# Optimization experiments

Hardware: AMD Instinct MI355X
Metric: run time of the kernel (lower is better)

The kernel has to match this reference:

```python
import jax, jax.numpy as jnp
import numpy as np

N = 50000      # num_nodes
E = 800000     # num_edges (avg degree 16)
F_IN = 128     # num_features
H = 64         # hidden dim (fixed in module code)
C = 16         # num_classes
R = 8          # num_relations
BN_EPS = 1e-5


def setup_inputs() -> dict:
    key = jax.random.key(0)
    ks = jax.random.split(key, 16)
    s = 0.05
    f32 = jnp.float32
    inp = {
        "x": jax.random.normal(ks[0], (N, F_IN), f32),
        "edge_index": jax.random.randint(ks[1], (2, E), 0, N, dtype=jnp.int32),
        "edge_type": jax.random.randint(ks[2], (E,), 0, R, dtype=jnp.int32),
        # RGCNConv layer 1: per-relation weights, root weight, bias
        "W1": jax.random.normal(ks[3], (R, F_IN, H), f32) * s,
        "root1": jax.random.normal(ks[4], (F_IN, H), f32) * s,
        "b1": jnp.zeros((H,), f32),
        # RGCNConv layer 2
        "W2": jax.random.normal(ks[5], (R, H, H), f32) * s,
        "root2": jax.random.normal(ks[6], (H, H), f32) * s,
        "b2": jnp.zeros((H,), f32),
        # RGCNConv layer 3
        "W3": jax.random.normal(ks[7], (R, H, H), f32) * s,
        "root3": jax.random.normal(ks[8], (H, H), f32) * s,
        "b3": jnp.zeros((H,), f32),
        # BatchNorm1d params + running stats (eval mode)
        "gamma1": jnp.ones((H,), f32), "beta1": jnp.zeros((H,), f32),
        "rm1": jnp.zeros((H,), f32),   "rv1": jnp.ones((H,), f32),
        "gamma2": jnp.ones((H,), f32), "beta2": jnp.zeros((H,), f32),
        "rm2": jnp.zeros((H,), f32),   "rv2": jnp.ones((H,), f32),
        "gamma3": jnp.ones((H,), f32), "beta3": jnp.zeros((H,), f32),
        "rm3": jnp.zeros((H,), f32),   "rv3": jnp.ones((H,), f32),
        # final linear
        "Wl": jax.random.normal(ks[9], (H, C), f32) * s,
        "bl": jnp.zeros((C,), f32),
    }
    return inp


def _rgcn(x, src, dst, edge_type, W, root, bias):
    # RGCNConv with mean aggregation per relation (PyG default):
    # out_i = x_i @ root + bias + sum_r mean_{j in N_r(i)} (x_j @ W_r)
    out = x @ root + bias
    for r in range(R):  # small fixed loop over relations
        h = x @ W[r]                      # [N, H] node-level transform
        mask = (edge_type == r)
        msg = jnp.where(mask[:, None], h[src], 0.0)   # [E, H]
        agg = jax.ops.segment_sum(msg, dst, num_segments=N)   # [N, H]
        cnt = jax.ops.segment_sum(mask.astype(x.dtype), dst, num_segments=N)
        out = out + agg / jnp.maximum(cnt, 1.0)[:, None]
    return out


def _bn(x, gamma, beta, rm, rv):
    # BatchNorm1d in eval mode with running stats
    return (x - rm) * jax.lax.rsqrt(rv + BN_EPS) * gamma + beta


def reference(x, edge_index, edge_type,
              W1, root1, b1, W2, root2, b2, W3, root3, b3,
              gamma1, beta1, rm1, rv1,
              gamma2, beta2, rm2, rv2,
              gamma3, beta3, rm3, rv3,
              Wl, bl):
    src, dst = edge_index[0], edge_index[1]
    h = jax.nn.relu(_rgcn(x, src, dst, edge_type, W1, root1, b1))
    h = _bn(h, gamma1, beta1, rm1, rv1)  # dropout = identity in eval
    h = jax.nn.relu(_rgcn(h, src, dst, edge_type, W2, root2, b2))
    h = _bn(h, gamma2, beta2, rm2, rv2)
    h = jax.nn.relu(_rgcn(h, src, dst, edge_type, W3, root3, b3))
    h = _bn(h, gamma3, beta3, rm3, rv3)
    return h @ Wl + bl  # [N, C]
```

## Files before the change

### kernel.cpp

```cpp
#include <hip/hip_runtime.h>


#define R_REL 8

typedef unsigned short ushort_t;
typedef short short8 __attribute__((ext_vector_type(8)));
typedef float f32x4 __attribute__((ext_vector_type(4)));

#define MFMA(a, b, c) __builtin_amdgcn_mfma_f32_16x16x32_bf16(a, b, c, 0, 0, 0)

static __device__ __forceinline__ unsigned short f2bf(float f) {
    unsigned int u = __float_as_uint(f);
    u = (u + 0x7FFF + ((u >> 16) & 1)) >> 16;
    return (unsigned short)u;
}
static __device__ __forceinline__ float bf2f(unsigned short h) {
    return __uint_as_float(((unsigned int)h) << 16);
}

__global__ void wcvt_kernel(const float* __restrict__ src, ushort_t* __restrict__ dst,
                            int G, int K)
{
    int i = blockIdx.x * 256 + threadIdx.x;
    if (i >= G * K * 64) return;
    int g = i / (K * 64), rem = i % (K * 64), k = rem >> 6, c = rem & 63;
    dst[(size_t)g * 64 * K + (size_t)c * K + k] = f2bf(src[i]);
}

__global__ void xcvt_kernel(const float* __restrict__ src, ushort_t* __restrict__ dst, int n4)
{
    int i = blockIdx.x * 256 + threadIdx.x;
    if (i >= n4) return;
    float4 v = ((const float4*)src)[i];
    ushort_t t[4] = {f2bf(v.x), f2bf(v.y), f2bf(v.z), f2bf(v.w)};
    *(uint2*)&dst[(size_t)i * 4] = *(const uint2*)t;
}

__global__ __launch_bounds__(256)
void mgemm_kernel(const ushort_t* __restrict__ A, int n, int K,
                  const ushort_t* __restrict__ WT, const ushort_t* __restrict__ RT,
                  const float* __restrict__ bias,
                  ushort_t* __restrict__ H, float* __restrict__ accb)
{
    __shared__ ushort_t As[64][136];
    __shared__ ushort_t Bs[64][136];

    const int row0 = blockIdx.x * 64;
    const int yr = blockIdx.y;
    const ushort_t* Bsrc = (yr < R_REL) ? (WT + (size_t)yr * 64 * K) : RT;

    const int tid = threadIdx.x;
    const int KB = K >> 3;

    for (int i = tid; i < 64 * KB; i += 256) {
        int r = i / KB, k8 = (i % KB) << 3;
        *(uint4*)&Bs[r][k8] = *(const uint4*)&Bsrc[(size_t)r * K + k8];
        uint4 av = make_uint4(0u, 0u, 0u, 0u);
        if (row0 + r < n) av = *(const uint4*)&A[(size_t)(row0 + r) * K + k8];
        *(uint4*)&As[r][k8] = av;
    }
    __syncthreads();

    const int wid  = tid >> 6;
    const int lane = tid & 63;
    const int wr = (wid >> 1) * 32;
    const int wc = (wid & 1) * 32;
    const int fr = lane & 15;
    const int kg = (lane >> 4) << 3;

    f32x4 acc[2][2] = {};
    for (int k0 = 0; k0 < K; k0 += 32) {
        short8 a0 = *(const short8*)&As[wr + fr     ][k0 + kg];
        short8 a1 = *(const short8*)&As[wr + 16 + fr][k0 + kg];
        short8 b0 = *(const short8*)&Bs[wc + fr     ][k0 + kg];
        short8 b1 = *(const short8*)&Bs[wc + 16 + fr][k0 + kg];
        acc[0][0] = MFMA(a0, b0, acc[0][0]);
        acc[0][1] = MFMA(a0, b1, acc[0][1]);
        acc[1][0] = MFMA(a1, b0, acc[1][0]);
        acc[1][1] = MFMA(a1, b1, acc[1][1]);
    }
    __syncthreads();

    float* Ct = (float*)As;
    const int rbase = (lane >> 4) << 2;
    #pragma unroll
    for (int m = 0; m < 2; ++m)
        #pragma unroll
        for (int nn = 0; nn < 2; ++nn)
            #pragma unroll
            for (int j = 0; j < 4; ++j)
                Ct[(wr + m * 16 + rbase + j) * 68 + wc + nn * 16 + fr] = acc[m][nn][j];
    __syncthreads();

    if (yr < R_REL) {
        const int cb = yr << 6;
        for (int i = tid; i < 64 * 8; i += 256) {
            int r = i >> 3, c8 = (i & 7) << 3;
            if (row0 + r < n) {
                ushort_t t[8];
                #pragma unroll
                for (int j = 0; j < 8; ++j) t[j] = f2bf(Ct[r * 68 + c8 + j]);
                *(uint4*)&H[(size_t)(row0 + r) * 512 + cb + c8] = *(const uint4*)t;
            }
        }
    } else {
        for (int i = tid; i < 64 * 16; i += 256) {
            int r = i >> 4, c4 = (i & 15) << 2;
            if (row0 + r < n) {
                float4 o;
                o.x = Ct[r * 68 + c4 + 0] + bias[c4 + 0];
                o.y = Ct[r * 68 + c4 + 1] + bias[c4 + 1];
                o.z = Ct[r * 68 + c4 + 2] + bias[c4 + 2];
                o.w = Ct[r * 68 + c4 + 3] + bias[c4 + 3];
                *(float4*)&accb[(size_t)(row0 + r) * 64 + c4] = o;
            }
        }
    }
}

__global__ void count_kernel(const int* __restrict__ ei, const int* __restrict__ et,
                             int* __restrict__ cnt, int E)
{
    int e = blockIdx.x * 256 + threadIdx.x;
    if (e < E) atomicAdd(&cnt[(size_t)ei[E + e] * R_REL + et[e]], 1);
}

__global__ void invdeg_kernel(float* __restrict__ inv, int* __restrict__ deg, int N)
{
    int i = blockIdx.x * 256 + threadIdx.x;
    if (i >= N) return;
    const int* c = (const int*)inv;
    int tot = 0;
    float out[R_REL];
    #pragma unroll
    for (int r = 0; r < R_REL; ++r) {
        int cc = c[i * R_REL + r];
        tot += cc;
        out[r] = 1.0f / (float)(cc > 1 ? cc : 1);
    }
    #pragma unroll
    for (int r = 0; r < R_REL; ++r) inv[i * R_REL + r] = out[r];
    deg[i] = tot;
}

__global__ void scan1_kernel(const int* __restrict__ deg, int* __restrict__ offs,
                             int* __restrict__ partials, int N)
{
    __shared__ int sm[256];
    int i = blockIdx.x * 256 + threadIdx.x;
    int c = (i < N) ? deg[i] : 0;
    sm[threadIdx.x] = c;
    __syncthreads();
    for (int off = 1; off < 256; off <<= 1) {
        int t = (threadIdx.x >= off) ? sm[threadIdx.x - off] : 0;
        __syncthreads();
        sm[threadIdx.x] += t;
        __syncthreads();
    }
    if (i < N) offs[i] = sm[threadIdx.x] - c;
    if (threadIdx.x == 255) partials[blockIdx.x] = sm[255];
}

__global__ void scan2_kernel(int* __restrict__ partials, int P)
{
    __shared__ int sm[256];
    __shared__ int carry;
    if (threadIdx.x == 0) carry = 0;
    __syncthreads();
    for (int base = 0; base < P; base += 256) {
        int i = base + threadIdx.x;
        int c = (i < P) ? partials[i] : 0;
        sm[threadIdx.x] = c;
        __syncthreads();
        for (int off = 1; off < 256; off <<= 1) {
            int t = (threadIdx.x >= off) ? sm[threadIdx.x - off] : 0;
            __syncthreads();
            sm[threadIdx.x] += t;
            __syncthreads();
        }
        int incl = sm[threadIdx.x];
        int cold = carry;
        if (i < P) partials[i] = incl - c + cold;
        __syncthreads();
        if (threadIdx.x == 0) carry = cold + sm[255];
        __syncthreads();
    }
}

__global__ void scan3_kernel(int* __restrict__ offs, const int* __restrict__ partials, int N)
{
    int i = blockIdx.x * 256 + threadIdx.x;
    if (i < N) offs[i] += partials[blockIdx.x];
}

__global__ void fill3_kernel(const int* __restrict__ ei, const int* __restrict__ et,
                             const int* __restrict__ offs, int* __restrict__ cursor,
                             const float* __restrict__ inv,
                             int2* __restrict__ ep, int E)
{
    int e = blockIdx.x * 256 + threadIdx.x;
    if (e >= E) return;
    int d = ei[E + e];
    int r = et[e];
    int pos = offs[d] + atomicAdd(&cursor[d], 1);
    ep[pos] = make_int2(ei[e] * 512 + r * 64,
                        __float_as_int(inv[(size_t)d * R_REL + r]));
}

__global__ __launch_bounds__(256)
void agg3_kernel(const int2* __restrict__ ep,
                 const int* __restrict__ offs, const int* __restrict__ deg,
                 const ushort_t* __restrict__ H, const float* __restrict__ accb,
                 const float* __restrict__ g, const float* __restrict__ b,
                 const float* __restrict__ rm, const float* __restrict__ rv,
                 ushort_t* __restrict__ xout, int N)
{
    const int lane = threadIdx.x & 63;
    const int d = (blockIdx.x * 256 + threadIdx.x) >> 6;
    if (d >= N) return;

    const int sub = lane >> 4;
    const int fl  = lane & 15;
    const int n0 = offs[d];
    const int dg = deg[d];

    float s0 = 0.f, s1 = 0.f, s2 = 0.f, s3 = 0.f;
    int k = 0;

    for (; k + 8 <= dg; k += 8) {
        int2 eA = ep[n0 + k + sub];
        int2 eB = ep[n0 + k + 4 + sub];
        uint2 hA = *(const uint2*)&H[(size_t)eA.x + (fl << 2)];
        uint2 hB = *(const uint2*)&H[(size_t)eB.x + (fl << 2)];
        float wA = __int_as_float(eA.y);
        float wB = __int_as_float(eB.y);
        s0 += bf2f((ushort_t)(hA.x & 0xFFFF)) * wA + bf2f((ushort_t)(hB.x & 0xFFFF)) * wB;
        s1 += bf2f((ushort_t)(hA.x >> 16))    * wA + bf2f((ushort_t)(hB.x >> 16))    * wB;
        s2 += bf2f((ushort_t)(hA.y & 0xFFFF)) * wA + bf2f((ushort_t)(hB.y & 0xFFFF)) * wB;
        s3 += bf2f((ushort_t)(hA.y >> 16))    * wA + bf2f((ushort_t)(hB.y >> 16))    * wB;
    }
    for (; k + 4 <= dg; k += 4) {
        int2 eA = ep[n0 + k + sub];
        uint2 hA = *(const uint2*)&H[(size_t)eA.x + (fl << 2)];
        float wA = __int_as_float(eA.y);
        s0 += bf2f((ushort_t)(hA.x & 0xFFFF)) * wA;
        s1 += bf2f((ushort_t)(hA.x >> 16))    * wA;
        s2 += bf2f((ushort_t)(hA.y & 0xFFFF)) * wA;
        s3 += bf2f((ushort_t)(hA.y >> 16))    * wA;
    }
    if (k < dg && sub < dg - k) {
        int2 eA = ep[n0 + k + sub];
        uint2 hA = *(const uint2*)&H[(size_t)eA.x + (fl << 2)];
        float wA = __int_as_float(eA.y);
        s0 += bf2f((ushort_t)(hA.x & 0xFFFF)) * wA;
        s1 += bf2f((ushort_t)(hA.x >> 16))    * wA;
        s2 += bf2f((ushort_t)(hA.y & 0xFFFF)) * wA;
        s3 += bf2f((ushort_t)(hA.y >> 16))    * wA;
    }

    s0 += __shfl_xor(s0, 16); s1 += __shfl_xor(s1, 16);
    s2 += __shfl_xor(s2, 16); s3 += __shfl_xor(s3, 16);
    s0 += __shfl_xor(s0, 32); s1 += __shfl_xor(s1, 32);
    s2 += __shfl_xor(s2, 32); s3 += __shfl_xor(s3, 32);

    if (sub == 0) {
        const int c4 = fl << 2;
        float4 a  = *(const float4*)&accb[(size_t)d * 64 + c4];
        float4 gm = *(const float4*)&g[c4];
        float4 bt = *(const float4*)&b[c4];
        float4 mu = *(const float4*)&rm[c4];
        float4 vr = *(const float4*)&rv[c4];
        float t0 = a.x + s0, t1 = a.y + s1, t2 = a.z + s2, t3 = a.w + s3;
        t0 = t0 > 0.f ? t0 : 0.f;  t1 = t1 > 0.f ? t1 : 0.f;
        t2 = t2 > 0.f ? t2 : 0.f;  t3 = t3 > 0.f ? t3 : 0.f;
        t0 = (t0 - mu.x) * rsqrtf(vr.x + 1e-5f) * gm.x + bt.x;
        t1 = (t1 - mu.y) * rsqrtf(vr.y + 1e-5f) * gm.y + bt.y;
        t2 = (t2 - mu.z) * rsqrtf(vr.z + 1e-5f) * gm.z + bt.z;
        t3 = (t3 - mu.w) * rsqrtf(vr.w + 1e-5f) * gm.w + bt.w;
        ushort_t o[4] = {f2bf(t0), f2bf(t1), f2bf(t2), f2bf(t3)};
        *(uint2*)&xout[(size_t)d * 64 + c4] = *(const uint2*)o;
    }
}

__global__ __launch_bounds__(256)
void lin_kernel(const ushort_t* __restrict__ h, const float* __restrict__ Wl,
                const float* __restrict__ bl, float* __restrict__ out, int N)
{
    __shared__ float w[64 * 16];
    __shared__ float bb[16];
    for (int i = threadIdx.x; i < 64 * 16; i += 256) w[i] = Wl[i];
    if (threadIdx.x < 16) bb[threadIdx.x] = bl[threadIdx.x];
    __syncthreads();

    int idx = blockIdx.x * 256 + threadIdx.x;
    if (idx >= N * 16) return;
    int node = idx >> 4, c = idx & 15;
    float s = bb[c];
    const ushort_t* hr = h + (size_t)node * 64;
    #pragma unroll 16
    for (int k = 0; k < 64; ++k) s += bf2f(hr[k]) * w[k * 16 + c];
    out[idx] = s;
}

extern "C" void kernel_launch(void* const* d_in, const int* in_sizes, int n_in,
                              void* d_out, int out_size, void* d_ws, size_t ws_size,
                              hipStream_t stream)
{
    const float* x  = (const float*)d_in[0];
    const int*   ei = (const int*)d_in[1];
    const int*   et = (const int*)d_in[2];
    const float* W[3]    = {(const float*)d_in[3], (const float*)d_in[6], (const float*)d_in[9]};
    const float* root[3] = {(const float*)d_in[4], (const float*)d_in[7], (const float*)d_in[10]};
    const float* bias[3] = {(const float*)d_in[5], (const float*)d_in[8], (const float*)d_in[11]};
    const float* gamma[3] = {(const float*)d_in[12], (const float*)d_in[16], (const float*)d_in[20]};
    const float* beta[3]  = {(const float*)d_in[13], (const float*)d_in[17], (const float*)d_in[21]};
    const float* rm[3]    = {(const float*)d_in[14], (const float*)d_in[18], (const float*)d_in[22]};
    const float* rv[3]    = {(const float*)d_in[15], (const float*)d_in[19], (const float*)d_in[23]};
    const float* Wl = (const float*)d_in[24];
    const float* bl = (const float*)d_in[25];

    const int N = in_sizes[0] / 128;
    const int E = in_sizes[2];
    const int K1 = 128;

    char* p = (char*)d_ws;
    float*   inv  = (float*)p;    p += (size_t)N * R_REL * 4;
    ushort_t* Hbuf = (ushort_t*)p; p += (size_t)N * 512 * 2;
    float*   accb = (float*)p;    p += (size_t)N * 64 * 4;
    ushort_t* xb  = (ushort_t*)p; p += (size_t)N * 64 * 2;
    ushort_t* x16 = (ushort_t*)p; p += (size_t)N * K1 * 2;
    ushort_t* wt0 = (ushort_t*)p; p += (size_t)R_REL * 64 * K1 * 2;
    ushort_t* wt1 = (ushort_t*)p; p += (size_t)R_REL * 64 * 64 * 2;
    ushort_t* wt2 = (ushort_t*)p; p += (size_t)R_REL * 64 * 64 * 2;
    ushort_t* rt0 = (ushort_t*)p; p += (size_t)64 * K1 * 2;
    ushort_t* rt1 = (ushort_t*)p; p += (size_t)64 * 64 * 2;
    ushort_t* rt2 = (ushort_t*)p; p += (size_t)64 * 64 * 2;
    int*   offs    = (int*)p;     p += (size_t)N * 4;
    int*   deg     = (int*)p;     p += (size_t)N * 4;
    int*   cursor  = (int*)p;     p += (size_t)N * 4;
    int2*  ep      = (int2*)p;    p += (size_t)E * 8;
    int*   partials = (int*)p;

    const ushort_t* wt[3] = {wt0, wt1, wt2};
    const ushort_t* rt[3] = {rt0, rt1, rt2};

    const int gxN = (N + 255) / 256;

    wcvt_kernel<<<(R_REL * K1 * 64 + 255) / 256, 256, 0, stream>>>(W[0], wt0, R_REL, K1);
    wcvt_kernel<<<(R_REL * 64 * 64 + 255) / 256, 256, 0, stream>>>(W[1], wt1, R_REL, 64);
    wcvt_kernel<<<(R_REL * 64 * 64 + 255) / 256, 256, 0, stream>>>(W[2], wt2, R_REL, 64);
    wcvt_kernel<<<(K1 * 64 + 255) / 256, 256, 0, stream>>>(root[0], rt0, 1, K1);
    wcvt_kernel<<<(64 * 64 + 255) / 256, 256, 0, stream>>>(root[1], rt1, 1, 64);
    wcvt_kernel<<<(64 * 64 + 255) / 256, 256, 0, stream>>>(root[2], rt2, 1, 64);
    xcvt_kernel<<<((N * K1 / 4) + 255) / 256, 256, 0, stream>>>(x, x16, N * K1 / 4);

    hipMemsetAsync(inv, 0, (size_t)N * R_REL * 4, stream);
    hipMemsetAsync(cursor, 0, (size_t)N * 4, stream);
    count_kernel<<<(E + 255) / 256, 256, 0, stream>>>(ei, et, (int*)inv, E);
    invdeg_kernel<<<gxN, 256, 0, stream>>>(inv, deg, N);
    scan1_kernel<<<gxN, 256, 0, stream>>>(deg, offs, partials, N);
    scan2_kernel<<<1, 256, 0, stream>>>(partials, gxN);
    scan3_kernel<<<gxN, 256, 0, stream>>>(offs, partials, N);
    fill3_kernel<<<(E + 255) / 256, 256, 0, stream>>>(ei, et, offs, cursor, inv, ep, E);

    const int gx = (N + 63) / 64;
    const int gagg = (N * 64 + 255) / 256;
    const ushort_t* cur = x16;
    for (int layer = 0; layer < 3; ++layer) {
        const int K = (layer == 0) ? K1 : 64;
        mgemm_kernel<<<dim3(gx, R_REL + 1), 256, 0, stream>>>(
            cur, N, K, wt[layer], rt[layer], bias[layer], Hbuf, accb);
        agg3_kernel<<<gagg, 256, 0, stream>>>(
            ep, offs, deg, Hbuf, accb,
            gamma[layer], beta[layer], rm[layer], rv[layer], xb, N);
        cur = xb;
    }

    lin_kernel<<<(N * 16 + 255) / 256, 256, 0, stream>>>(cur, Wl, bl, (float*)d_out, N);
}
```

Baseline: 396.5 us.

## Restructure GEMM to reuse A across relations, pack edges, fuse final linear

The relation GEMM now loads each block's A rows into registers once and loops over all 9 weight matrices, reading B directly from global memory instead of staging through LDS. Results are written straight from the MFMA accumulators, with the bias folded into the initial accumulator. Edge records shrink from 8 to 4 bytes by packing src and relation into one int and looking up the inverse degree per destination at aggregation time. The six weight-conversion launches become one, and the final linear layer is fused into the last aggregation kernel via shuffles. The packing assumes node ids fit in 16 bits, which holds for N=50000.

```diff
diff --git a/kernel.cpp b/kernel.cpp
--- a/kernel.cpp
+++ b/kernel.cpp
@@ -18,13 +18,22 @@
     return __uint_as_float(((unsigned int)h) << 16);
 }
 
-__global__ void wcvt_kernel(const float* __restrict__ src, ushort_t* __restrict__ dst,
-                            int G, int K)
+struct WcvtA {
+    const float* src[6];
+    ushort_t*    dst[6];
+    int          end[6];
+    int          K[6];
+};
+__global__ void wcvt6_kernel(WcvtA a, int total)
 {
     int i = blockIdx.x * 256 + threadIdx.x;
-    if (i >= G * K * 64) return;
-    int g = i / (K * 64), rem = i % (K * 64), k = rem >> 6, c = rem & 63;
-    dst[(size_t)g * 64 * K + (size_t)c * K + k] = f2bf(src[i]);
+    if (i >= total) return;
+    int s = 0;
+    while (i >= a.end[s]) ++s;
+    int j = i - (s ? a.end[s - 1] : 0);
+    int K = a.K[s];
+    int g = j / (K * 64), rem = j % (K * 64), k = rem >> 6, c = rem & 63;
+    a.dst[s][(size_t)g * 64 * K + (size_t)c * K + k] = f2bf(a.src[s][j]);
 }
 
 __global__ void xcvt_kernel(const float* __restrict__ src, ushort_t* __restrict__ dst, int n4)
@@ -36,83 +45,85 @@
     *(uint2*)&dst[(size_t)i * 4] = *(const uint2*)t;
 }
 
+template<int K>
 __global__ __launch_bounds__(256)
-void mgemm_kernel(const ushort_t* __restrict__ A, int n, int K,
-                  const ushort_t* __restrict__ WT, const ushort_t* __restrict__ RT,
-                  const float* __restrict__ bias,
-                  ushort_t* __restrict__ H, float* __restrict__ accb)
-{
-    __shared__ ushort_t As[64][136];
-    __shared__ ushort_t Bs[64][136];
-
-    const int row0 = blockIdx.x * 64;
-    const int yr = blockIdx.y;
-    const ushort_t* Bsrc = (yr < R_REL) ? (WT + (size_t)yr * 64 * K) : RT;
-
+void mgemm2_kernel(const ushort_t* __restrict__ A, int n,
+                   const ushort_t* __restrict__ WT, const ushort_t* __restrict__ RT,
+                   const float* __restrict__ bias,
+                   ushort_t* __restrict__ H, float* __restrict__ accb)
+{
+    constexpr int KS = K / 32;
     const int tid = threadIdx.x;
-    const int KB = K >> 3;
-
-    for (int i = tid; i < 64 * KB; i += 256) {
-        int r = i / KB, k8 = (i % KB) << 3;
-        *(uint4*)&Bs[r][k8] = *(const uint4*)&Bsrc[(size_t)r * K + k8];
-        uint4 av = make_uint4(0u, 0u, 0u, 0u);
-        if (row0 + r < n) av = *(const uint4*)&A[(size_t)(row0 + r) * K + k8];
-        *(uint4*)&As[r][k8] = av;
-    }
-    __syncthreads();
-
-    const int wid  = tid >> 6;
-    const int lane = tid & 63;
-    const int wr = (wid >> 1) * 32;
-    const int wc = (wid & 1) * 32;
+    const int wid = tid >> 6, lane = tid & 63;
+    const int wr = (wid >> 1) << 5;
+    const int wc = (wid & 1) << 5;
     const int fr = lane & 15;
     const int kg = (lane >> 4) << 3;
-
-    f32x4 acc[2][2] = {};
-    for (int k0 = 0; k0 < K; k0 += 32) {
-        short8 a0 = *(const short8*)&As[wr + fr     ][k0 + kg];
-        short8 a1 = *(const short8*)&As[wr + 16 + fr][k0 + kg];
-        short8 b0 = *(const short8*)&Bs[wc + fr     ][k0 + kg];
-        short8 b1 = *(const short8*)&Bs[wc + 16 + fr][k0 + kg];
-        acc[0][0] = MFMA(a0, b0, acc[0][0]);
-        acc[0][1] = MFMA(a0, b1, acc[0][1]);
-        acc[1][0] = MFMA(a1, b0, acc[1][0]);
-        acc[1][1] = MFMA(a1, b1, acc[1][1]);
-    }
-    __syncthreads();
-
-    float* Ct = (float*)As;
-    const int rbase = (lane >> 4) << 2;
+    const int cq = (lane >> 4) << 2;
+    const int row0 = blockIdx.x * 64;
+
+    short8 a[2][KS];
     #pragma unroll
-    for (int m = 0; m < 2; ++m)
+    for (int m = 0; m < 2; ++m) {
+        int rr = row0 + wr + m * 16 + fr;
+        if (rr < n) {
+            #pragma unroll
+            for (int ks = 0; ks < KS; ++ks)
+                a[m][ks] = *(const short8*)&A[(size_t)rr * K + ks * 32 + kg];
+        } else {
+            #pragma unroll
+            for (int ks = 0; ks < KS; ++ks)
+                a[m][ks] = short8{0, 0, 0, 0, 0, 0, 0, 0};
+        }
+    }
+
+    for (int r = 0; r < 9; ++r) {
+        const ushort_t* B = (r < R_REL) ? (WT + (size_t)r * 64 * K) : RT;
+
+        short8 b[2][KS];
         #pragma unroll
         for (int nn = 0; nn < 2; ++nn)
             #pragma unroll
-            for (int j = 0; j < 4; ++j)
-                Ct[(wr + m * 16 + rbase + j) * 68 + wc + nn * 16 + fr] = acc[m][nn][j];
-    __syncthreads();
-
-    if (yr < R_REL) {
-        const int cb = yr << 6;
-        for (int i = tid; i < 64 * 8; i += 256) {
-            int r = i >> 3, c8 = (i & 7) << 3;
-            if (row0 + r < n) {
-                ushort_t t[8];
+            for (int ks = 0; ks < KS; ++ks)
+                b[nn][ks] = *(const short8*)&B[(size_t)(wc + nn * 16 + fr) * K + ks * 32 + kg];
+
+        f32x4 acc[2][2];
+        if (r == R_REL) {
+            #pragma unroll
+            for (int nn = 0; nn < 2; ++nn) {
+                float4 bv = *(const float4*)&bias[wc + nn * 16 + cq];
+                acc[nn][0] = f32x4{bv.x, bv.y, bv.z, bv.w};
+                acc[nn][1] = acc[nn][0];
+            }
+        } else {
+            acc[0][0] = f32x4{0.f, 0.f, 0.f, 0.f};
+            acc[0][1] = acc[0][0]; acc[1][0] = acc[0][0]; acc[1][1] = acc[0][0];
+        }
+
+        #pragma unroll
+        for (int ks = 0; ks < KS; ++ks)
+            #pragma unroll
+            for (int nn = 0; nn < 2; ++nn)
                 #pragma unroll
-                for (int j = 0; j < 8; ++j) t[j] = f2bf(Ct[r * 68 + c8 + j]);
-                *(uint4*)&H[(size_t)(row0 + r) * 512 + cb + c8] = *(const uint4*)t;
-            }
-        }
-    } else {
-        for (int i = tid; i < 64 * 16; i += 256) {
-            int r = i >> 4, c4 = (i & 15) << 2;
-            if (row0 + r < n) {
-                float4 o;
-                o.x = Ct[r * 68 + c4 + 0] + bias[c4 + 0];
-                o.y = Ct[r * 68 + c4 + 1] + bias[c4 + 1];
-                o.z = Ct[r * 68 + c4 + 2] + bias[c4 + 2];
-                o.w = Ct[r * 68 + c4 + 3] + bias[c4 + 3];
-                *(float4*)&accb[(size_t)(row0 + r) * 64 + c4] = o;
+                for (int m = 0; m < 2; ++m)
+                    acc[nn][m] = MFMA(b[nn][ks], a[m][ks], acc[nn][m]);
+
+        #pragma unroll
+        for (int m = 0; m < 2; ++m) {
+            int rr = row0 + wr + m * 16 + fr;
+            if (rr >= n) continue;
+            #pragma unroll
+            for (int nn = 0; nn < 2; ++nn) {
+                if (r < R_REL) {
+                    ushort_t t[4] = {f2bf(acc[nn][m][0]), f2bf(acc[nn][m][1]),
+                                     f2bf(acc[nn][m][2]), f2bf(acc[nn][m][3])};
+                    *(uint2*)&H[(size_t)rr * 512 + (r << 6) + wc + nn * 16 + cq] =
+                        *(const uint2*)t;
+                } else {
+                    *(float4*)&accb[(size_t)rr * 64 + wc + nn * 16 + cq] =
+                        make_float4(acc[nn][m][0], acc[nn][m][1],
+                                    acc[nn][m][2], acc[nn][m][3]);
+                }
             }
         }
     }
@@ -193,27 +204,27 @@
     if (i < N) offs[i] += partials[blockIdx.x];
 }
 
-__global__ void fill3_kernel(const int* __restrict__ ei, const int* __restrict__ et,
+__global__ void fill4_kernel(const int* __restrict__ ei, const int* __restrict__ et,
                              const int* __restrict__ offs, int* __restrict__ cursor,
-                             const float* __restrict__ inv,
-                             int2* __restrict__ ep, int E)
+                             int* __restrict__ ep, int E)
 {
     int e = blockIdx.x * 256 + threadIdx.x;
     if (e >= E) return;
     int d = ei[E + e];
-    int r = et[e];
     int pos = offs[d] + atomicAdd(&cursor[d], 1);
-    ep[pos] = make_int2(ei[e] * 512 + r * 64,
-                        __float_as_int(inv[(size_t)d * R_REL + r]));
+    ep[pos] = ei[e] | (et[e] << 16);
 }
 
 __global__ __launch_bounds__(256)
-void agg3_kernel(const int2* __restrict__ ep,
+void agg4_kernel(const int* __restrict__ ep,
                  const int* __restrict__ offs, const int* __restrict__ deg,
                  const ushort_t* __restrict__ H, const float* __restrict__ accb,
+                 const float* __restrict__ inv,
                  const float* __restrict__ g, const float* __restrict__ b,
                  const float* __restrict__ rm, const float* __restrict__ rv,
-                 ushort_t* __restrict__ xout, int N)
+                 ushort_t* __restrict__ xout,
+                 const float* __restrict__ Wl, const float* __restrict__ bl,
+                 float* __restrict__ out, int N, int last)
 {
     const int lane = threadIdx.x & 63;
     const int d = (blockIdx.x * 256 + threadIdx.x) >> 6;
@@ -223,35 +234,36 @@
     const int fl  = lane & 15;
     const int n0 = offs[d];
     const int dg = deg[d];
+    const float* invd = &inv[(size_t)d * R_REL];
 
     float s0 = 0.f, s1 = 0.f, s2 = 0.f, s3 = 0.f;
     int k = 0;
 
     for (; k + 8 <= dg; k += 8) {
-        int2 eA = ep[n0 + k + sub];
-        int2 eB = ep[n0 + k + 4 + sub];
-        uint2 hA = *(const uint2*)&H[(size_t)eA.x + (fl << 2)];
-        uint2 hB = *(const uint2*)&H[(size_t)eB.x + (fl << 2)];
-        float wA = __int_as_float(eA.y);
-        float wB = __int_as_float(eB.y);
+        int pA = ep[n0 + k + sub];
+        int pB = ep[n0 + k + 4 + sub];
+        uint2 hA = *(const uint2*)&H[(size_t)(pA & 0xFFFF) * 512 + ((pA >> 16) << 6) + (fl << 2)];
+        uint2 hB = *(const uint2*)&H[(size_t)(pB & 0xFFFF) * 512 + ((pB >> 16) << 6) + (fl << 2)];
+        float wA = invd[pA >> 16];
+        float wB = invd[pB >> 16];
         s0 += bf2f((ushort_t)(hA.x & 0xFFFF)) * wA + bf2f((ushort_t)(hB.x & 0xFFFF)) * wB;
         s1 += bf2f((ushort_t)(hA.x >> 16))    * wA + bf2f((ushort_t)(hB.x >> 16))    * wB;
         s2 += bf2f((ushort_t)(hA.y & 0xFFFF)) * wA + bf2f((ushort_t)(hB.y & 0xFFFF)) * wB;
         s3 += bf2f((ushort_t)(hA.y >> 16))    * wA + bf2f((ushort_t)(hB.y >> 16))    * wB;
     }
     for (; k + 4 <= dg; k += 4) {
-        int2 eA = ep[n0 + k + sub];
-        uint2 hA = *(const uint2*)&H[(size_t)eA.x + (fl << 2)];
-        float wA = __int_as_float(eA.y);
+        int pA = ep[n0 + k + sub];
+        uint2 hA = *(const uint2*)&H[(size_t)(pA & 0xFFFF) * 512 + ((pA >> 16) << 6) + (fl << 2)];
+        float wA = invd[pA >> 16];
         s0 += bf2f((ushort_t)(hA.x & 0xFFFF)) * wA;
         s1 += bf2f((ushort_t)(hA.x >> 16))    * wA;
         s2 += bf2f((ushort_t)(hA.y & 0xFFFF)) * wA;
         s3 += bf2f((ushort_t)(hA.y >> 16))    * wA;
     }
     if (k < dg && sub < dg - k) {
-        int2 eA = ep[n0 + k + sub];
-        uint2 hA = *(const uint2*)&H[(size_t)eA.x + (fl << 2)];
-        float wA = __int_as_float(eA.y);
+        int pA = ep[n0 + k + sub];
+        uint2 hA = *(const uint2*)&H[(size_t)(pA & 0xFFFF) * 512 + ((pA >> 16) << 6) + (fl << 2)];
+        float wA = invd[pA >> 16];
         s0 += bf2f((ushort_t)(hA.x & 0xFFFF)) * wA;
         s1 += bf2f((ushort_t)(hA.x >> 16))    * wA;
         s2 += bf2f((ushort_t)(hA.y & 0xFFFF)) * wA;
@@ -263,43 +275,45 @@
     s0 += __shfl_xor(s0, 32); s1 += __shfl_xor(s1, 32);
     s2 += __shfl_xor(s2, 32); s3 += __shfl_xor(s3, 32);
 
-    if (sub == 0) {
-        const int c4 = fl << 2;
-        float4 a  = *(const float4*)&accb[(size_t)d * 64 + c4];
-        float4 gm = *(const float4*)&g[c4];
-        float4 bt = *(const float4*)&b[c4];
-        float4 mu = *(const float4*)&rm[c4];
-        float4 vr = *(const float4*)&rv[c4];
-        float t0 = a.x + s0, t1 = a.y + s1, t2 = a.z + s2, t3 = a.w + s3;
-        t0 = t0 > 0.f ? t0 : 0.f;  t1 = t1 > 0.f ? t1 : 0.f;
-        t2 = t2 > 0.f ? t2 : 0.f;  t3 = t3 > 0.f ? t3 : 0.f;
-        t0 = (t0 - mu.x) * rsqrtf(vr.x + 1e-5f) * gm.x + bt.x;
-        t1 = (t1 - mu.y) * rsqrtf(vr.y + 1e-5f) * gm.y + bt.y;
-        t2 = (t2 - mu.z) * rsqrtf(vr.z + 1e-5f) * gm.z + bt.z;
-        t3 = (t3 - mu.w) * rsqrtf(vr.w + 1e-5f) * gm.w + bt.w;
-        ushort_t o[4] = {f2bf(t0), f2bf(t1), f2bf(t2), f2bf(t3)};
-        *(uint2*)&xout[(size_t)d * 64 + c4] = *(const uint2*)o;
-    }
-}
-
-__global__ __launch_bounds__(256)
-void lin_kernel(const ushort_t* __restrict__ h, const float* __restrict__ Wl,
-                const float* __restrict__ bl, float* __restrict__ out, int N)
-{
-    __shared__ float w[64 * 16];
-    __shared__ float bb[16];
-    for (int i = threadIdx.x; i < 64 * 16; i += 256) w[i] = Wl[i];
-    if (threadIdx.x < 16) bb[threadIdx.x] = bl[threadIdx.x];
-    __syncthreads();
-
-    int idx = blockIdx.x * 256 + threadIdx.x;
-    if (idx >= N * 16) return;
-    int node = idx >> 4, c = idx & 15;
-    float s = bb[c];
-    const ushort_t* hr = h + (size_t)node * 64;
-    #pragma unroll 16
-    for (int k = 0; k < 64; ++k) s += bf2f(hr[k]) * w[k * 16 + c];
-    out[idx] = s;
+    const int c4 = fl << 2;
+    float4 aq = *(const float4*)&accb[(size_t)d * 64 + c4];
+    float4 gm = *(const float4*)&g[c4];
+    float4 bt = *(const float4*)&b[c4];
+    float4 mu = *(const float4*)&rm[c4];
+    float4 vr = *(const float4*)&rv[c4];
+    float t0 = aq.x + s0, t1 = aq.y + s1, t2 = aq.z + s2, t3 = aq.w + s3;
+    t0 = t0 > 0.f ? t0 : 0.f;  t1 = t1 > 0.f ? t1 : 0.f;
+    t2 = t2 > 0.f ? t2 : 0.f;  t3 = t3 > 0.f ? t3 : 0.f;
+    t0 = (t0 - mu.x) * rsqrtf(vr.x + 1e-5f) * gm.x + bt.x;
+    t1 = (t1 - mu.y) * rsqrtf(vr.y + 1e-5f) * gm.y + bt.y;
+    t2 = (t2 - mu.z) * rsqrtf(vr.z + 1e-5f) * gm.z + bt.z;
+    t3 = (t3 - mu.w) * rsqrtf(vr.w + 1e-5f) * gm.w + bt.w;
+
+    if (!last) {
+        if (sub == 0) {
+            ushort_t o[4] = {f2bf(t0), f2bf(t1), f2bf(t2), f2bf(t3)};
+            *(uint2*)&xout[(size_t)d * 64 + c4] = *(const uint2*)o;
+        }
+    } else {
+        float p0 = 0.f, p1 = 0.f, p2 = 0.f, p3 = 0.f;
+        float tt[4] = {t0, t1, t2, t3};
+        #pragma unroll
+        for (int i = 0; i < 4; ++i) {
+            float4 wv = *(const float4*)&Wl[(size_t)(c4 + i) * 16 + (sub << 2)];
+            p0 += tt[i] * wv.x; p1 += tt[i] * wv.y;
+            p2 += tt[i] * wv.z; p3 += tt[i] * wv.w;
+        }
+        #pragma unroll
+        for (int m = 1; m < 16; m <<= 1) {
+            p0 += __shfl_xor(p0, m); p1 += __shfl_xor(p1, m);
+            p2 += __shfl_xor(p2, m); p3 += __shfl_xor(p3, m);
+        }
+        if (fl == 0) {
+            float4 bv = *(const float4*)&bl[sub << 2];
+            *(float4*)&out[(size_t)d * 16 + (sub << 2)] =
+                make_float4(p0 + bv.x, p1 + bv.y, p2 + bv.z, p3 + bv.w);
+        }
+    }
 }
 
 extern "C" void kernel_launch(void* const* d_in, const int* in_sizes, int n_in,
@@ -338,7 +352,7 @@
     int*   offs    = (int*)p;     p += (size_t)N * 4;
     int*   deg     = (int*)p;     p += (size_t)N * 4;
     int*   cursor  = (int*)p;     p += (size_t)N * 4;
-    int2*  ep      = (int2*)p;    p += (size_t)E * 8;
+    int*   ep      = (int*)p;     p += (size_t)E * 4;
     int*   partials = (int*)p;
 
     const ushort_t* wt[3] = {wt0, wt1, wt2};
@@ -346,12 +360,20 @@
 
     const int gxN = (N + 255) / 256;
 
-    wcvt_kernel<<<(R_REL * K1 * 64 + 255) / 256, 256, 0, stream>>>(W[0], wt0, R_REL, K1);
-    wcvt_kernel<<<(R_REL * 64 * 64 + 255) / 256, 256, 0, stream>>>(W[1], wt1, R_REL, 64);
-    wcvt_kernel<<<(R_REL * 64 * 64 + 255) / 256, 256, 0, stream>>>(W[2], wt2, R_REL, 64);
-    wcvt_kernel<<<(K1 * 64 + 255) / 256, 256, 0, stream>>>(root[0], rt0, 1, K1);
-    wcvt_kernel<<<(64 * 64 + 255) / 256, 256, 0, stream>>>(root[1], rt1, 1, 64);
-    wcvt_kernel<<<(64 * 64 + 255) / 256, 256, 0, stream>>>(root[2], rt2, 1, 64);
+    {
+        WcvtA a;
+        a.src[0] = W[0];   a.dst[0] = wt0; a.K[0] = K1;
+        a.src[1] = W[1];   a.dst[1] = wt1; a.K[1] = 64;
+        a.src[2] = W[2];   a.dst[2] = wt2; a.K[2] = 64;
+        a.src[3] = root[0]; a.dst[3] = rt0; a.K[3] = K1;
+        a.src[4] = root[1]; a.dst[4] = rt1; a.K[4] = 64;
+        a.src[5] = root[2]; a.dst[5] = rt2; a.K[5] = 64;
+        int sizes[6] = {R_REL * K1 * 64, R_REL * 64 * 64, R_REL * 64 * 64,
+                        K1 * 64, 64 * 64, 64 * 64};
+        int acc = 0;
+        for (int i = 0; i < 6; ++i) { acc += sizes[i]; a.end[i] = acc; }
+        wcvt6_kernel<<<(acc + 255) / 256, 256, 0, stream>>>(a, acc);
+    }
     xcvt_kernel<<<((N * K1 / 4) + 255) / 256, 256, 0, stream>>>(x, x16, N * K1 / 4);
 
     hipMemsetAsync(inv, 0, (size_t)N * R_REL * 4, stream);
@@ -361,20 +383,23 @@
     scan1_kernel<<<gxN, 256, 0, stream>>>(deg, offs, partials, N);
     scan2_kernel<<<1, 256, 0, stream>>>(partials, gxN);
     scan3_kernel<<<gxN, 256, 0, stream>>>(offs, partials, N);
-    fill3_kernel<<<(E + 255) / 256, 256, 0, stream>>>(ei, et, offs, cursor, inv, ep, E);
+    fill4_kernel<<<(E + 255) / 256, 256, 0, stream>>>(ei, et, offs, cursor, ep, E);
 
     const int gx = (N + 63) / 64;
     const int gagg = (N * 64 + 255) / 256;
     const ushort_t* cur = x16;
     for (int layer = 0; layer < 3; ++layer) {
-        const int K = (layer == 0) ? K1 : 64;
-        mgemm_kernel<<<dim3(gx, R_REL + 1), 256, 0, stream>>>(
-            cur, N, K, wt[layer], rt[layer], bias[layer], Hbuf, accb);
-        agg3_kernel<<<gagg, 256, 0, stream>>>(
-            ep, offs, deg, Hbuf, accb,
-            gamma[layer], beta[layer], rm[layer], rv[layer], xb, N);
+        if (layer == 0)
+            mgemm2_kernel<128><<<gx, 256, 0, stream>>>(
+                cur, N, wt[0], rt[0], bias[0], Hbuf, accb);
+        else
+            mgemm2_kernel<64><<<gx, 256, 0, stream>>>(
+                cur, N, wt[layer], rt[layer], bias[layer], Hbuf, accb);
+        int last = (layer == 2);
+        agg4_kernel<<<gagg, 256, 0, stream>>>(
+            ep, offs, deg, Hbuf, accb, inv,
+            gamma[layer], beta[layer], rm[layer], rv[layer],
+            xb, Wl, bl, (float*)d_out, N, last);
         cur = xb;
     }
-
-    lin_kernel<<<(N * 16 + 255) / 256, 256, 0, stream>>>(cur, Wl, bl, (float*)d_out, N);
-}
+}
```

New measurement: 427.0 us. 1.08x slower.

## Fuse conversions, scan, and final linear into neighboring kernels; template GEMM on K

Applied to the files above, without the earlier changes.

Merges the six weight-conversion launches into one, folds the x fp32-to-bf16 conversion into the layer-1 GEMM load, combines invdeg with the first scan stage, and fuses the final linear layer into the last aggregation kernel using lane shuffles. The GEMM is templated on K so its inner loop fully unrolls. The aim is to cut launch count and the extra HBM round trips for x16 and the last-layer activations. The fused linear layer adds shuffle reductions to the aggregation epilogue, and the GEMM now reads x as fp32, so twice the bytes per row for layer 1.

```diff
diff --git a/kernel.cpp b/kernel.cpp
--- a/kernel.cpp
+++ b/kernel.cpp
@@ -18,26 +18,27 @@
     return __uint_as_float(((unsigned int)h) << 16);
 }
 
-__global__ void wcvt_kernel(const float* __restrict__ src, ushort_t* __restrict__ dst,
-                            int G, int K)
+struct WcvtA {
+    const float* src[6];
+    ushort_t*    dst[6];
+    int          end[6];
+    int          K[6];
+};
+__global__ void wcvt6_kernel(WcvtA a, int total)
 {
     int i = blockIdx.x * 256 + threadIdx.x;
-    if (i >= G * K * 64) return;
-    int g = i / (K * 64), rem = i % (K * 64), k = rem >> 6, c = rem & 63;
-    dst[(size_t)g * 64 * K + (size_t)c * K + k] = f2bf(src[i]);
-}
-
-__global__ void xcvt_kernel(const float* __restrict__ src, ushort_t* __restrict__ dst, int n4)
-{
-    int i = blockIdx.x * 256 + threadIdx.x;
-    if (i >= n4) return;
-    float4 v = ((const float4*)src)[i];
-    ushort_t t[4] = {f2bf(v.x), f2bf(v.y), f2bf(v.z), f2bf(v.w)};
-    *(uint2*)&dst[(size_t)i * 4] = *(const uint2*)t;
-}
-
+    if (i >= total) return;
+    int s = 0;
+    while (i >= a.end[s]) ++s;
+    int j = i - (s ? a.end[s - 1] : 0);
+    int K = a.K[s];
+    int g = j / (K * 64), rem = j % (K * 64), k = rem >> 6, c = rem & 63;
+    a.dst[s][(size_t)g * 64 * K + (size_t)c * K + k] = f2bf(a.src[s][j]);
+}
+
+template<int K, bool AF32>
 __global__ __launch_bounds__(256)
-void mgemm_kernel(const ushort_t* __restrict__ A, int n, int K,
+void mgemm_kernel(const void* __restrict__ Av, int n,
                   const ushort_t* __restrict__ WT, const ushort_t* __restrict__ RT,
                   const float* __restrict__ bias,
                   ushort_t* __restrict__ H, float* __restrict__ accb)
@@ -55,20 +56,34 @@
     for (int i = tid; i < 64 * KB; i += 256) {
         int r = i / KB, k8 = (i % KB) << 3;
         *(uint4*)&Bs[r][k8] = *(const uint4*)&Bsrc[(size_t)r * K + k8];
-        uint4 av = make_uint4(0u, 0u, 0u, 0u);
-        if (row0 + r < n) av = *(const uint4*)&A[(size_t)(row0 + r) * K + k8];
-        *(uint4*)&As[r][k8] = av;
+        if (AF32) {
+            const float* Af = (const float*)Av;
+            float4 f0 = make_float4(0.f, 0.f, 0.f, 0.f), f1 = f0;
+            if (row0 + r < n) {
+                f0 = *(const float4*)&Af[(size_t)(row0 + r) * K + k8];
+                f1 = *(const float4*)&Af[(size_t)(row0 + r) * K + k8 + 4];
+            }
+            ushort_t t[8] = {f2bf(f0.x), f2bf(f0.y), f2bf(f0.z), f2bf(f0.w),
+                             f2bf(f1.x), f2bf(f1.y), f2bf(f1.z), f2bf(f1.w)};
+            *(uint4*)&As[r][k8] = *(const uint4*)t;
+        } else {
+            const ushort_t* Ab = (const ushort_t*)Av;
+            uint4 av = make_uint4(0u, 0u, 0u, 0u);
+            if (row0 + r < n) av = *(const uint4*)&Ab[(size_t)(row0 + r) * K + k8];
+            *(uint4*)&As[r][k8] = av;
+        }
     }
     __syncthreads();
 
     const int wid  = tid >> 6;
     const int lane = tid & 63;
-    const int wr = (wid >> 1) * 32;
-    const int wc = (wid & 1) * 32;
+    const int wr = (wid >> 1) << 5;
+    const int wc = (wid & 1) << 5;
     const int fr = lane & 15;
     const int kg = (lane >> 4) << 3;
 
     f32x4 acc[2][2] = {};
+    #pragma unroll
     for (int k0 = 0; k0 < K; k0 += 32) {
         short8 a0 = *(const short8*)&As[wr + fr     ][k0 + kg];
         short8 a1 = *(const short8*)&As[wr + 16 + fr][k0 + kg];
@@ -125,31 +140,27 @@
     if (e < E) atomicAdd(&cnt[(size_t)ei[E + e] * R_REL + et[e]], 1);
 }
 
-__global__ void invdeg_kernel(float* __restrict__ inv, int* __restrict__ deg, int N)
-{
-    int i = blockIdx.x * 256 + threadIdx.x;
-    if (i >= N) return;
-    const int* c = (const int*)inv;
-    int tot = 0;
-    float out[R_REL];
-    #pragma unroll
-    for (int r = 0; r < R_REL; ++r) {
-        int cc = c[i * R_REL + r];
-        tot += cc;
-        out[r] = 1.0f / (float)(cc > 1 ? cc : 1);
-    }
-    #pragma unroll
-    for (int r = 0; r < R_REL; ++r) inv[i * R_REL + r] = out[r];
-    deg[i] = tot;
-}
-
-__global__ void scan1_kernel(const int* __restrict__ deg, int* __restrict__ offs,
-                             int* __restrict__ partials, int N)
+__global__ void invdeg_scan_kernel(float* __restrict__ inv, int* __restrict__ deg,
+                                   int* __restrict__ offs, int* __restrict__ partials,
+                                   int N)
 {
     __shared__ int sm[256];
     int i = blockIdx.x * 256 + threadIdx.x;
-    int c = (i < N) ? deg[i] : 0;
-    sm[threadIdx.x] = c;
+    int tot = 0;
+    if (i < N) {
+        const int* c = (const int*)inv;
+        float out[R_REL];
+        #pragma unroll
+        for (int r = 0; r < R_REL; ++r) {
+            int cc = c[(size_t)i * R_REL + r];
+            tot += cc;
+            out[r] = 1.0f / (float)(cc > 1 ? cc : 1);
+        }
+        #pragma unroll
+        for (int r = 0; r < R_REL; ++r) inv[(size_t)i * R_REL + r] = out[r];
+        deg[i] = tot;
+    }
+    sm[threadIdx.x] = tot;
     __syncthreads();
     for (int off = 1; off < 256; off <<= 1) {
         int t = (threadIdx.x >= off) ? sm[threadIdx.x - off] : 0;
@@ -157,7 +168,7 @@
         sm[threadIdx.x] += t;
         __syncthreads();
     }
-    if (i < N) offs[i] = sm[threadIdx.x] - c;
+    if (i < N) offs[i] = sm[threadIdx.x] - tot;
     if (threadIdx.x == 255) partials[blockIdx.x] = sm[255];
 }
 
@@ -208,12 +219,14 @@
 }
 
 __global__ __launch_bounds__(256)
-void agg3_kernel(const int2* __restrict__ ep,
+void agg5_kernel(const int2* __restrict__ ep,
                  const int* __restrict__ offs, const int* __restrict__ deg,
                  const ushort_t* __restrict__ H, const float* __restrict__ accb,
                  const float* __restrict__ g, const float* __restrict__ b,
                  const float* __restrict__ rm, const float* __restrict__ rv,
-                 ushort_t* __restrict__ xout, int N)
+                 ushort_t* __restrict__ xout,
+                 const float* __restrict__ Wl, const float* __restrict__ bl,
+                 float* __restrict__ out, int N, int last)
 {
     const int lane = threadIdx.x & 63;
     const int d = (blockIdx.x * 256 + threadIdx.x) >> 6;
@@ -265,41 +278,52 @@
 
     if (sub == 0) {
         const int c4 = fl << 2;
-        float4 a  = *(const float4*)&accb[(size_t)d * 64 + c4];
+        float4 aq = *(const float4*)&accb[(size_t)d * 64 + c4];
         float4 gm = *(const float4*)&g[c4];
         float4 bt = *(const float4*)&b[c4];
         float4 mu = *(const float4*)&rm[c4];
         float4 vr = *(const float4*)&rv[c4];
-        float t0 = a.x + s0, t1 = a.y + s1, t2 = a.z + s2, t3 = a.w + s3;
+        float t0 = aq.x + s0, t1 = aq.y + s1, t2 = aq.z + s2, t3 = aq.w + s3;
         t0 = t0 > 0.f ? t0 : 0.f;  t1 = t1 > 0.f ? t1 : 0.f;
         t2 = t2 > 0.f ? t2 : 0.f;  t3 = t3 > 0.f ? t3 : 0.f;
         t0 = (t0 - mu.x) * rsqrtf(vr.x + 1e-5f) * gm.x + bt.x;
         t1 = (t1 - mu.y) * rsqrtf(vr.y + 1e-5f) * gm.y + bt.y;
         t2 = (t2 - mu.z) * rsqrtf(vr.z + 1e-5f) * gm.z + bt.z;
         t3 = (t3 - mu.w) * rsqrtf(vr.w + 1e-5f) * gm.w + bt.w;
-        ushort_t o[4] = {f2bf(t0), f2bf(t1), f2bf(t2), f2bf(t3)};
-        *(uint2*)&xout[(size_t)d * 64 + c4] = *(const uint2*)o;
-    }
-}
-
-__global__ __launch_bounds__(256)
-void lin_kernel(const ushort_t* __restrict__ h, const float* __restrict__ Wl,
-                const float* __restrict__ bl, float* __restrict__ out, int N)
-{
-    __shared__ float w[64 * 16];
-    __shared__ float bb[16];
-    for (int i = threadIdx.x; i < 64 * 16; i += 256) w[i] = Wl[i];
-    if (threadIdx.x < 16) bb[threadIdx.x] = bl[threadIdx.x];
-    __syncthreads();
-
-    int idx = blockIdx.x * 256 + threadIdx.x;
-    if (idx >= N * 16) return;
-    int node = idx >> 4, c = idx & 15;
-    float s = bb[c];
-    const ushort_t* hr = h + (size_t)node * 64;
-    #pragma unroll 16
-    for (int k = 0; k < 64; ++k) s += bf2f(hr[k]) * w[k * 16 + c];
-    out[idx] = s;
+
+        if (!last) {
+            ushort_t o[4] = {f2bf(t0), f2bf(t1), f2bf(t2), f2bf(t3)};
+            *(uint2*)&xout[(size_t)d * 64 + c4] = *(const uint2*)o;
+        } else {
+            f32x4 p[4] = {};
+            float tt[4] = {t0, t1, t2, t3};
+            #pragma unroll
+            for (int i = 0; i < 4; ++i) {
+                const float* wrow = &Wl[(size_t)(c4 + i) * 16];
+                #pragma unroll
+                for (int q = 0; q < 4; ++q)
+                    p[q] += tt[i] * (*(const f32x4*)&wrow[q * 4]);
+            }
+            #pragma unroll
+            for (int m = 1; m < 16; m <<= 1) {
+                #pragma unroll
+                for (int q = 0; q < 4; ++q) {
+                    p[q][0] += __shfl_xor(p[q][0], m);
+                    p[q][1] += __shfl_xor(p[q][1], m);
+                    p[q][2] += __shfl_xor(p[q][2], m);
+                    p[q][3] += __shfl_xor(p[q][3], m);
+                }
+            }
+            if (fl == 0) {
+                #pragma unroll
+                for (int q = 0; q < 4; ++q) {
+                    f32x4 bv = *(const f32x4*)&bl[q * 4];
+                    f32x4 o = p[q] + bv;
+                    *(f32x4*)&out[(size_t)d * 16 + q * 4] = o;
+                }
+            }
+        }
+    }
 }
 
 extern "C" void kernel_launch(void* const* d_in, const int* in_sizes, int n_in,
@@ -328,7 +352,6 @@
     ushort_t* Hbuf = (ushort_t*)p; p += (size_t)N * 512 * 2;
     float*   accb = (float*)p;    p += (size_t)N * 64 * 4;
     ushort_t* xb  = (ushort_t*)p; p += (size_t)N * 64 * 2;
-    ushort_t* x16 = (ushort_t*)p; p += (size_t)N * K1 * 2;
     ushort_t* wt0 = (ushort_t*)p; p += (size_t)R_REL * 64 * K1 * 2;
     ushort_t* wt1 = (ushort_t*)p; p += (size_t)R_REL * 64 * 64 * 2;
     ushort_t* wt2 = (ushort_t*)p; p += (size_t)R_REL * 64 * 64 * 2;
@@ -346,35 +369,44 @@
 
     const int gxN = (N + 255) / 256;
 
-    wcvt_kernel<<<(R_REL * K1 * 64 + 255) / 256, 256, 0, stream>>>(W[0], wt0, R_REL, K1);
-    wcvt_kernel<<<(R_REL * 64 * 64 + 255) / 256, 256, 0, stream>>>(W[1], wt1, R_REL, 64);
-    wcvt_kernel<<<(R_REL * 64 * 64 + 255) / 256, 256, 0, stream>>>(W[2], wt2, R_REL, 64);
-    wcvt_kernel<<<(K1 * 64 + 255) / 256, 256, 0, stream>>>(root[0], rt0, 1, K1);
-    wcvt_kernel<<<(64 * 64 + 255) / 256, 256, 0, stream>>>(root[1], rt1, 1, 64);
-    wcvt_kernel<<<(64 * 64 + 255) / 256, 256, 0, stream>>>(root[2], rt2, 1, 64);
-    xcvt_kernel<<<((N * K1 / 4) + 255) / 256, 256, 0, stream>>>(x, x16, N * K1 / 4);
+    {
+        WcvtA a;
+        a.src[0] = W[0];   a.dst[0] = wt0; a.K[0] = K1;
+        a.src[1] = W[1];   a.dst[1] = wt1; a.K[1] = 64;
+        a.src[2] = W[2];   a.dst[2] = wt2; a.K[2] = 64;
+        a.src[3] = root[0]; a.dst[3] = rt0; a.K[3] = K1;
+        a.src[4] = root[1]; a.dst[4] = rt1; a.K[4] = 64;
+        a.src[5] = root[2]; a.dst[5] = rt2; a.K[5] = 64;
+        int sizes[6] = {R_REL * K1 * 64, R_REL * 64 * 64, R_REL * 64 * 64,
+                        K1 * 64, 64 * 64, 64 * 64};
+        int acc = 0;
+        for (int i = 0; i < 6; ++i) { acc += sizes[i]; a.end[i] = acc; }
+        wcvt6_kernel<<<(acc + 255) / 256, 256, 0, stream>>>(a, acc);
+    }
 
     hipMemsetAsync(inv, 0, (size_t)N * R_REL * 4, stream);
     hipMemsetAsync(cursor, 0, (size_t)N * 4, stream);
     count_kernel<<<(E + 255) / 256, 256, 0, stream>>>(ei, et, (int*)inv, E);
-    invdeg_kernel<<<gxN, 256, 0, stream>>>(inv, deg, N);
-    scan1_kernel<<<gxN, 256, 0, stream>>>(deg, offs, partials, N);
+    invdeg_scan_kernel<<<gxN, 256, 0, stream>>>(inv, deg, offs, partials, N);
     scan2_kernel<<<1, 256, 0, stream>>>(partials, gxN);
     scan3_kernel<<<gxN, 256, 0, stream>>>(offs, partials, N);
     fill3_kernel<<<(E + 255) / 256, 256, 0, stream>>>(ei, et, offs, cursor, inv, ep, E);
 
     const int gx = (N + 63) / 64;
     const int gagg = (N * 64 + 255) / 256;
-    const ushort_t* cur = x16;
+    const ushort_t* cur = nullptr;
     for (int layer = 0; layer < 3; ++layer) {
-        const int K = (layer == 0) ? K1 : 64;
-        mgemm_kernel<<<dim3(gx, R_REL + 1), 256, 0, stream>>>(
-            cur, N, K, wt[layer], rt[layer], bias[layer], Hbuf, accb);
-        agg3_kernel<<<gagg, 256, 0, stream>>>(
+        if (layer == 0)
+            mgemm_kernel<128, true><<<dim3(gx, R_REL + 1), 256, 0, stream>>>(
+                (const void*)x, N, wt[0], rt[0], bias[0], Hbuf, accb);
+        else
+            mgemm_kernel<64, false><<<dim3(gx, R_REL + 1), 256, 0, stream>>>(
+                (const void*)cur, N, wt[layer], rt[layer], bias[layer], Hbuf, accb);
+        int last = (layer == 2);
+        agg5_kernel<<<gagg, 256, 0, stream>>>(
             ep, offs, deg, Hbuf, accb,
-            gamma[layer], beta[layer], rm[layer], rv[layer], xb, N);
+            gamma[layer], beta[layer], rm[layer], rv[layer],
+            xb, Wl, bl, (float*)d_out, N, last);
         cur = xb;
     }
-
-    lin_kernel<<<(N * 16 + 255) / 256, 256, 0, stream>>>(cur, Wl, bl, (float*)d_out, N);
-}
+}
```

Measured after the change: 413.3 us. +4.2%, slower.
